# Optimization experiments

Measured on AMD Instinct MI355X. Metric: run time of the kernel, lower is better.

## Reference

```python
import jax, jax.numpy as jnp
import numpy as np

D_MODEL = 1024


def setup_inputs() -> dict:
    key = jax.random.key(0)
    kx, kq, kk, kv = jax.random.split(key, 4)
    x = jax.random.normal(kx, (4, 2048, D_MODEL), dtype=jnp.float32)
    s = 1.0 / np.sqrt(D_MODEL)
    # torch nn.Linear weight is [out, in]; y = x @ W.T
    Wq = jax.random.normal(kq, (D_MODEL, D_MODEL), dtype=jnp.float32) * s
    Wk = jax.random.normal(kk, (D_MODEL, D_MODEL), dtype=jnp.float32) * s
    Wv = jax.random.normal(kv, (D_MODEL, D_MODEL), dtype=jnp.float32) * s
    return {"x": x, "Wq": Wq, "Wk": Wk, "Wv": Wv}


def reference(x, Wq, Wk, Wv):
    # Linear projections (no bias): [b, s, d]
    Q = jnp.einsum("bsd,ed->bse", x, Wq)
    K = jnp.einsum("bsd,ed->bse", x, Wk)
    V = jnp.einsum("bsd,ed->bse", x, Wv)
    d_k = Q.shape[-1]
    scores = jnp.einsum("bqd,bkd->bqk", Q, K) / jnp.sqrt(jnp.asarray(d_k, Q.dtype))
    weights = jax.nn.softmax(scores, axis=-1)
    return jnp.einsum("bqk,bkd->bqd", weights, V)
```

## Files before the change

### kernel.cpp

```cpp
#include <hip/hip_runtime.h>
#include <hip/hip_bf16.h>

using bf16 = __hip_bfloat16;
typedef __attribute__((ext_vector_type(8))) short short8;
typedef __attribute__((ext_vector_type(16))) float f32x16;

__global__ __launch_bounds__(256) void cast_all(const float* __restrict__ x,
                                                const float* __restrict__ Wq,
                                                const float* __restrict__ Wk,
                                                const float* __restrict__ Wv,
                                                bf16* __restrict__ xb, bf16* __restrict__ Wb) {
  const int b = blockIdx.x;
  const float* src;
  bf16* dst;
  if (b < 8192) {
    src = x + (size_t)b * 1024;
    dst = xb + (size_t)b * 1024;
  } else if (b < 9216) {
    src = Wq + (size_t)(b - 8192) * 1024;
    dst = Wb + (size_t)(b - 8192) * 1024;
  } else if (b < 10240) {
    src = Wk + (size_t)(b - 9216) * 1024;
    dst = Wb + (size_t)(b - 8192) * 1024;
  } else {
    src = Wv + (size_t)(b - 10240) * 1024;
    dst = Wb + (size_t)(b - 8192) * 1024;
  }
  const int i = threadIdx.x * 4;
  const float4 f = *(const float4*)(src + i);
  bf16 h[4];
  h[0] = __float2bfloat16(f.x);
  h[1] = __float2bfloat16(f.y);
  h[2] = __float2bfloat16(f.z);
  h[3] = __float2bfloat16(f.w);
  *(uint2*)(dst + i) = *(const uint2*)h;
}

template <int BK, int SMEM_BYTES, class Epi>
__device__ __forceinline__ void gemm_nt(const bf16* __restrict__ A, const bf16* __restrict__ B,
                                        int lda, int ldb, int K, int m0, int n0, Epi epi) {
  constexpr int KS = BK / 16;
  constexpr int CPR = BK / 8;
  constexpr int SH = (BK == 32) ? 2 : 3;
  constexpr int N_INSTR = 128 * CPR / 256;
  constexpr int BUFB = 128 * BK * 2 * 2;
  static_assert(2 * BUFB <= SMEM_BYTES, "need two staging buffers");
  __shared__ char smem[SMEM_BYTES];
  const int t = threadIdx.x;
  const int lane = t & 63;
  const int wave = t >> 6;
  const int wm = (wave >> 1) * 64;
  const int wn = (wave & 1) * 64;

  f32x16 acc[2][2];
#pragma unroll
  for (int i = 0; i < 2; ++i)
#pragma unroll
    for (int j = 0; j < 2; ++j)
#pragma unroll
      for (int r = 0; r < 16; ++r) acc[i][j][r] = 0.f;

  const bf16* gA[N_INSTR];
  const bf16* gB[N_INSTR];
#pragma unroll
  for (int j = 0; j < N_INSTR; ++j) {
    const int slot = j * 256 + t;
    const int row = slot >> SH;
    const int f = (row + (row >> SH)) & (CPR - 1);
    const int c = ((slot & (CPR - 1)) ^ f) << 3;
    gA[j] = A + (size_t)(m0 + row) * lda + c;
    gB[j] = B + (size_t)(n0 + row) * ldb + c;
  }

  const int rl = lane & 31;
  const int grp = lane >> 5;

  auto stage = [&](int k0, int buf) {
    char* base = smem + buf * BUFB;
    bf16* As = (bf16*)base;
    bf16* Bs = (bf16*)(base + 128 * BK * 2);
#pragma unroll
    for (int j = 0; j < N_INSTR; ++j) {
      __builtin_amdgcn_global_load_lds(
          (const __attribute__((address_space(1))) unsigned int*)(gA[j] + k0),
          (__attribute__((address_space(3))) unsigned int*)(As + (j * 256 + wave * 64) * 8), 16, 0, 0);
      __builtin_amdgcn_global_load_lds(
          (const __attribute__((address_space(1))) unsigned int*)(gB[j] + k0),
          (__attribute__((address_space(3))) unsigned int*)(Bs + (j * 256 + wave * 64) * 8), 16, 0, 0);
    }
  };

  const int NT = K / BK;

  stage(0, 0);
  stage(BK, 1);
  asm volatile("s_waitcnt vmcnt(8)" ::: "memory");
  __builtin_amdgcn_s_barrier();
  __builtin_amdgcn_sched_barrier(0);

  for (int kt = 0; kt < NT; ++kt) {
    const char* base = smem + (kt & 1) * BUFB;
    const bf16* As = (const bf16*)base;
    const bf16* Bs = (const bf16*)(base + 128 * BK * 2);

    short8 af[KS][2], bv[KS][2];
#pragma unroll
    for (int ks = 0; ks < KS; ++ks) {
      const int kb = ks * 2 + grp;
#pragma unroll
      for (int mt = 0; mt < 2; ++mt) {
        const int rowa = wm + mt * 32 + rl;
        const int fa = (rowa + (rowa >> SH)) & (CPR - 1);
        af[ks][mt] = *(const short8*)(As + rowa * BK + ((kb ^ fa) << 3));
        const int rowb = wn + mt * 32 + rl;
        const int fb = (rowb + (rowb >> SH)) & (CPR - 1);
        bv[ks][mt] = *(const short8*)(Bs + rowb * BK + ((kb ^ fb) << 3));
      }
    }
    __builtin_amdgcn_sched_barrier(0);
    asm volatile("s_waitcnt lgkmcnt(0)" ::: "memory");
    __builtin_amdgcn_sched_barrier(0);
    __builtin_amdgcn_s_barrier();
    __builtin_amdgcn_sched_barrier(0);

    if (kt + 2 < NT) stage((kt + 2) * BK, kt & 1);

    __builtin_amdgcn_s_setprio(1);
#pragma unroll
    for (int ks = 0; ks < KS; ++ks)
#pragma unroll
      for (int mt = 0; mt < 2; ++mt)
#pragma unroll
        for (int nt = 0; nt < 2; ++nt)
          acc[mt][nt] = __builtin_amdgcn_mfma_f32_32x32x16_bf16(af[ks][mt], bv[ks][nt],
                                                                acc[mt][nt], 0, 0, 0);
    __builtin_amdgcn_s_setprio(0);
    __builtin_amdgcn_sched_barrier(0);

    if (kt + 1 < NT) {
      if (kt + 2 < NT) {
        asm volatile("s_waitcnt vmcnt(8)" ::: "memory");
      } else {
        asm volatile("s_waitcnt vmcnt(0)" ::: "memory");
      }
      __builtin_amdgcn_s_barrier();
      __builtin_amdgcn_sched_barrier(0);
    }
  }
  __syncthreads();

  epi(acc, m0, n0, wm, wn, lane, wave, smem);
}

__device__ __forceinline__ int c_row(int reg, int lane) {
  return (reg & 3) + 8 * (reg >> 2) + 4 * (lane >> 5);
}

template <class F>
__device__ __forceinline__ void for_each_c(const f32x16 (&acc)[2][2], int wm, int wn, int lane,
                                           F f) {
  const int rl = lane & 31;
#pragma unroll
  for (int mt = 0; mt < 2; ++mt)
#pragma unroll
    for (int nt = 0; nt < 2; ++nt)
#pragma unroll
      for (int reg = 0; reg < 16; ++reg)
        f(wm + mt * 32 + c_row(reg, lane), wn + nt * 32 + rl, acc[mt][nt][reg]);
}

__global__ __launch_bounds__(256) void proj_kernel(const bf16* __restrict__ xb,
                                                   const bf16* __restrict__ Wb,
                                                   bf16* __restrict__ Qb, bf16* __restrict__ Kb,
                                                   bf16* __restrict__ Vt) {
  const int id = blockIdx.y * 24 + blockIdx.x;
  const int g = id & 7, s = id >> 3;
  const int m0 = (g * 8 + (s & 7)) * 128;
  const int n0 = (s >> 3) * 128;
  gemm_nt<64, 65536>(xb, Wb, 1024, 1024, 1024, m0, n0,
             [=](const f32x16 (&acc)[2][2], int m0, int n0, int wm, int wn, int lane, int wave,
                 char* smem) {
    if (n0 < 2048) {
      bf16* dst = (n0 < 1024) ? Qb : Kb;
      const int nb = (n0 < 1024) ? n0 : (n0 - 1024);
      for_each_c(acc, wm, wn, lane, [&](int m, int n, float v) {
        dst[(size_t)(m0 + m) * 1024 + nb + n] = __float2bfloat16(v);
      });
    } else {
      bf16* T = (bf16*)(smem) + wave * 2304;
      const int rl = lane & 31;
      const int g4 = 4 * (lane >> 5);
      const int mbase = m0 + wm;
      const int bb = mbase >> 11;
      const int sbase = mbase & 2047;
      const int nvbase = n0 - 2048 + wn;
#pragma unroll
      for (int p = 0; p < 2; ++p) {
#pragma unroll
        for (int mt = 0; mt < 2; ++mt)
#pragma unroll
          for (int q = 0; q < 4; ++q) {
            bf16 h4[4];
#pragma unroll
            for (int r = 0; r < 4; ++r) h4[r] = __float2bfloat16(acc[mt][p][4 * q + r]);
            *(uint2*)(T + rl * 72 + mt * 32 + 8 * q + g4) = *(const uint2*)h4;
          }
        asm volatile("s_waitcnt lgkmcnt(0)" ::: "memory");
#pragma unroll
        for (int i = 0; i < 4; ++i) {
          const int nl = i * 8 + (lane >> 3);
          const int ml = (lane & 7) * 8;
          const short8 val = *(const short8*)(T + nl * 72 + ml);
          *(short8*)(Vt + ((size_t)bb * 1024 + nvbase + p * 32 + nl) * 2048 + sbase + ml) = val;
        }
        asm volatile("s_waitcnt lgkmcnt(0)" ::: "memory");
      }
    }
  });
}

__global__ __launch_bounds__(256) void qk_exp_kernel(const bf16* __restrict__ Qb,
                                                     const bf16* __restrict__ Kb,
                                                     bf16* __restrict__ E,
                                                     float* __restrict__ Lpart) {
  const int z = blockIdx.z;
  const int id2 = blockIdx.y * 16 + blockIdx.x;
  const int g = id2 & 7, s = id2 >> 3;
  const int m0 = ((g & 3) * 4 + (s & 3)) * 128;
  const int n0 = ((g >> 2) * 8 + (s >> 2)) * 128;
  const bf16* A = Qb + (size_t)z * 2048 * 1024;
  const bf16* B = Kb + (size_t)z * 2048 * 1024;
  bf16* Ez = E + (size_t)z * 2048 * 2048;
  float* Lz = Lpart + (size_t)z * 16 * 2048;
  gemm_nt<64, 65536>(A, B, 1024, 1024, 1024, m0, n0,
             [=](const f32x16 (&acc)[2][2], int m0, int n0, int wm, int wn, int lane, int wave,
                 char* smem) {
    float* Lp = (float*)smem;
    const int rl = lane & 31;
#pragma unroll
    for (int mt = 0; mt < 2; ++mt)
#pragma unroll
      for (int reg = 0; reg < 16; ++reg) {
        const int mr = wm + mt * 32 + c_row(reg, lane);
        float s2 = 0.f;
#pragma unroll
        for (int nt = 0; nt < 2; ++nt) {
          const float e = __expf(acc[mt][nt][reg] * 0.03125f);
          Ez[(size_t)(m0 + mr) * 2048 + n0 + wn + nt * 32 + rl] = __float2bfloat16(e);
          s2 += e;
        }
        s2 += __shfl_xor(s2, 1, 64);
        s2 += __shfl_xor(s2, 2, 64);
        s2 += __shfl_xor(s2, 4, 64);
        s2 += __shfl_xor(s2, 8, 64);
        s2 += __shfl_xor(s2, 16, 64);
        if (rl == 0) Lp[mr * 2 + (wave & 1)] = s2;
      }
    __syncthreads();
    const int t = threadIdx.x;
    if (t < 128) Lz[(n0 >> 7) * 2048 + m0 + t] = Lp[t * 2 + 0] + Lp[t * 2 + 1];
  });
}

__global__ __launch_bounds__(256) void pv_kernel(const bf16* __restrict__ E,
                                                 const bf16* __restrict__ Vt,
                                                 const float* __restrict__ Lpart,
                                                 float* __restrict__ out) {
  const int z = blockIdx.z;
  const int id2 = blockIdx.y * 8 + blockIdx.x;
  const int g = id2 & 7, s = id2 >> 3;
  const int m0 = ((g & 3) * 4 + (s & 3)) * 128;
  const int n0 = ((g >> 2) * 4 + (s >> 2)) * 128;
  const bf16* A = E + (size_t)z * 2048 * 2048;
  const bf16* B = Vt + (size_t)z * 1024 * 2048;
  const float* Lz = Lpart + (size_t)z * 16 * 2048;
  float* oz = out + (size_t)z * 2048 * 1024;
  gemm_nt<64, 65536>(A, B, 2048, 2048, 2048, m0, n0,
             [=](const f32x16 (&acc)[2][2], int m0, int n0, int wm, int wn, int lane, int wave,
                 char* smem) {
    float* Lsm = (float*)smem;
    const int t = threadIdx.x;
    if (t < 128) {
      float s2 = 0.f;
#pragma unroll
      for (int i = 0; i < 16; ++i) s2 += Lz[(size_t)i * 2048 + m0 + t];
      Lsm[t] = 1.f / s2;
    }
    __syncthreads();
    const int rl = lane & 31;
#pragma unroll
    for (int mt = 0; mt < 2; ++mt)
#pragma unroll
      for (int reg = 0; reg < 16; ++reg) {
        const int ml = wm + mt * 32 + c_row(reg, lane);
        const float il = Lsm[ml];
#pragma unroll
        for (int nt = 0; nt < 2; ++nt)
          oz[(size_t)(m0 + ml) * 1024 + n0 + wn + nt * 32 + rl] = acc[mt][nt][reg] * il;
      }
  });
}

extern "C" void kernel_launch(void* const* d_in, const int* in_sizes, int n_in,
                              void* d_out, int out_size, void* d_ws, size_t ws_size,
                              hipStream_t stream) {
  const float* x = (const float*)d_in[0];
  const float* Wq = (const float*)d_in[1];
  const float* Wk = (const float*)d_in[2];
  const float* Wv = (const float*)d_in[3];
  float* out = (float*)d_out;

  char* w = (char*)d_ws;
  bf16* xb = (bf16*)w; w += (size_t)8192 * 1024 * 2;
  bf16* Wb = (bf16*)w; w += (size_t)3072 * 1024 * 2;
  bf16* Qb = (bf16*)w; w += (size_t)8192 * 1024 * 2;
  bf16* Kb = (bf16*)w; w += (size_t)8192 * 1024 * 2;
  bf16* Vt = (bf16*)w; w += (size_t)8192 * 1024 * 2;
  bf16* E  = (bf16*)w; w += (size_t)4 * 2048 * 2048 * 2;
  float* Lpart = (float*)w; w += (size_t)4 * 16 * 2048 * 4;

  cast_all<<<11264, 256, 0, stream>>>(x, Wq, Wk, Wv, xb, Wb);

  proj_kernel<<<dim3(24, 64), 256, 0, stream>>>(xb, Wb, Qb, Kb, Vt);

  qk_exp_kernel<<<dim3(16, 16, 4), 256, 0, stream>>>(Qb, Kb, E, Lpart);

  pv_kernel<<<dim3(8, 16, 4), 256, 0, stream>>>(E, Vt, Lpart, out);
}
```

Before: 240.7 us.

## Shrink GEMM K-tile to 32 with single-barrier double buffering and occupancy 4

Hardcodes the shared GEMM core to BK=32 with two 16KB LDS slots. It also replaces the two-stage-ahead prefetch, which had split vmcnt waits and two barriers per iteration, with a one-ahead prefetch issued right after the fragment loads and followed by a full vmcnt(0) wait and a single barrier. All three GEMM kernels now request four blocks per CU via launch_bounds, which the smaller LDS footprint makes possible. The aim is to hide latency through occupancy rather than deep in-block prefetch, at the cost of shorter K steps, more barriers per unit of work, and less prefetch distance per block.

Result: slower. 248.5 us (+3.3%).

```diff
diff --git a/kernel.cpp b/kernel.cpp
--- a/kernel.cpp
+++ b/kernel.cpp
@@ -36,16 +36,15 @@
   *(uint2*)(dst + i) = *(const uint2*)h;
 }
 
-template <int BK, int SMEM_BYTES, class Epi>
+template <class Epi>
 __device__ __forceinline__ void gemm_nt(const bf16* __restrict__ A, const bf16* __restrict__ B,
                                         int lda, int ldb, int K, int m0, int n0, Epi epi) {
-  constexpr int KS = BK / 16;
-  constexpr int CPR = BK / 8;
-  constexpr int SH = (BK == 32) ? 2 : 3;
-  constexpr int N_INSTR = 128 * CPR / 256;
-  constexpr int BUFB = 128 * BK * 2 * 2;
-  static_assert(2 * BUFB <= SMEM_BYTES, "need two staging buffers");
-  __shared__ char smem[SMEM_BYTES];
+  constexpr int BK = 32;
+  constexpr int CPR = 4;
+  constexpr int SH = 2;
+  constexpr int N_INSTR = 2;
+  constexpr int SLOT = 128 * BK * 2 * 2;
+  __shared__ char smem[2 * SLOT];
   const int t = threadIdx.x;
   const int lane = t & 63;
   const int wave = t >> 6;
@@ -75,10 +74,11 @@
   const int rl = lane & 31;
   const int grp = lane >> 5;
 
-  auto stage = [&](int k0, int buf) {
-    char* base = smem + buf * BUFB;
+  auto stage = [&](int kt) {
+    char* base = smem + (kt & 1) * SLOT;
     bf16* As = (bf16*)base;
     bf16* Bs = (bf16*)(base + 128 * BK * 2);
+    const int k0 = kt * BK;
 #pragma unroll
     for (int j = 0; j < N_INSTR; ++j) {
       __builtin_amdgcn_global_load_lds(
@@ -90,22 +90,21 @@
     }
   };
 
-  const int NT = K / BK;
-
-  stage(0, 0);
-  stage(BK, 1);
-  asm volatile("s_waitcnt vmcnt(8)" ::: "memory");
+  const int NT = K >> 5;
+
+  stage(0);
+  asm volatile("s_waitcnt vmcnt(0)" ::: "memory");
   __builtin_amdgcn_s_barrier();
   __builtin_amdgcn_sched_barrier(0);
 
   for (int kt = 0; kt < NT; ++kt) {
-    const char* base = smem + (kt & 1) * BUFB;
+    const char* base = smem + (kt & 1) * SLOT;
     const bf16* As = (const bf16*)base;
     const bf16* Bs = (const bf16*)(base + 128 * BK * 2);
 
-    short8 af[KS][2], bv[KS][2];
-#pragma unroll
-    for (int ks = 0; ks < KS; ++ks) {
+    short8 af[2][2], bv[2][2];
+#pragma unroll
+    for (int ks = 0; ks < 2; ++ks) {
       const int kb = ks * 2 + grp;
 #pragma unroll
       for (int mt = 0; mt < 2; ++mt) {
@@ -117,17 +116,14 @@
         bv[ks][mt] = *(const short8*)(Bs + rowb * BK + ((kb ^ fb) << 3));
       }
     }
+    if (kt + 1 < NT) stage(kt + 1);
+
     __builtin_amdgcn_sched_barrier(0);
     asm volatile("s_waitcnt lgkmcnt(0)" ::: "memory");
     __builtin_amdgcn_sched_barrier(0);
-    __builtin_amdgcn_s_barrier();
-    __builtin_amdgcn_sched_barrier(0);
-
-    if (kt + 2 < NT) stage((kt + 2) * BK, kt & 1);
-
     __builtin_amdgcn_s_setprio(1);
 #pragma unroll
-    for (int ks = 0; ks < KS; ++ks)
+    for (int ks = 0; ks < 2; ++ks)
 #pragma unroll
       for (int mt = 0; mt < 2; ++mt)
 #pragma unroll
@@ -136,16 +132,9 @@
                                                                 acc[mt][nt], 0, 0, 0);
     __builtin_amdgcn_s_setprio(0);
     __builtin_amdgcn_sched_barrier(0);
-
-    if (kt + 1 < NT) {
-      if (kt + 2 < NT) {
-        asm volatile("s_waitcnt vmcnt(8)" ::: "memory");
-      } else {
-        asm volatile("s_waitcnt vmcnt(0)" ::: "memory");
-      }
-      __builtin_amdgcn_s_barrier();
-      __builtin_amdgcn_sched_barrier(0);
-    }
+    asm volatile("s_waitcnt vmcnt(0)" ::: "memory");
+    __builtin_amdgcn_s_barrier();
+    __builtin_amdgcn_sched_barrier(0);
   }
   __syncthreads();
 
@@ -169,17 +158,18 @@
         f(wm + mt * 32 + c_row(reg, lane), wn + nt * 32 + rl, acc[mt][nt][reg]);
 }
 
-__global__ __launch_bounds__(256) void proj_kernel(const bf16* __restrict__ xb,
-                                                   const bf16* __restrict__ Wb,
-                                                   bf16* __restrict__ Qb, bf16* __restrict__ Kb,
-                                                   bf16* __restrict__ Vt) {
+__global__ __launch_bounds__(256, 4) void proj_kernel(const bf16* __restrict__ xb,
+                                                      const bf16* __restrict__ Wb,
+                                                      bf16* __restrict__ Qb,
+                                                      bf16* __restrict__ Kb,
+                                                      bf16* __restrict__ Vt) {
   const int id = blockIdx.y * 24 + blockIdx.x;
   const int g = id & 7, s = id >> 3;
   const int m0 = (g * 8 + (s & 7)) * 128;
   const int n0 = (s >> 3) * 128;
-  gemm_nt<64, 65536>(xb, Wb, 1024, 1024, 1024, m0, n0,
-             [=](const f32x16 (&acc)[2][2], int m0, int n0, int wm, int wn, int lane, int wave,
-                 char* smem) {
+  gemm_nt(xb, Wb, 1024, 1024, 1024, m0, n0,
+          [=](const f32x16 (&acc)[2][2], int m0, int n0, int wm, int wn, int lane, int wave,
+              char* smem) {
     if (n0 < 2048) {
       bf16* dst = (n0 < 1024) ? Qb : Kb;
       const int nb = (n0 < 1024) ? n0 : (n0 - 1024);
@@ -219,10 +209,10 @@
   });
 }
 
-__global__ __launch_bounds__(256) void qk_exp_kernel(const bf16* __restrict__ Qb,
-                                                     const bf16* __restrict__ Kb,
-                                                     bf16* __restrict__ E,
-                                                     float* __restrict__ Lpart) {
+__global__ __launch_bounds__(256, 4) void qk_exp_kernel(const bf16* __restrict__ Qb,
+                                                        const bf16* __restrict__ Kb,
+                                                        bf16* __restrict__ E,
+                                                        float* __restrict__ Lpart) {
   const int z = blockIdx.z;
   const int id2 = blockIdx.y * 16 + blockIdx.x;
   const int g = id2 & 7, s = id2 >> 3;
@@ -232,9 +222,9 @@
   const bf16* B = Kb + (size_t)z * 2048 * 1024;
   bf16* Ez = E + (size_t)z * 2048 * 2048;
   float* Lz = Lpart + (size_t)z * 16 * 2048;
-  gemm_nt<64, 65536>(A, B, 1024, 1024, 1024, m0, n0,
-             [=](const f32x16 (&acc)[2][2], int m0, int n0, int wm, int wn, int lane, int wave,
-                 char* smem) {
+  gemm_nt(A, B, 1024, 1024, 1024, m0, n0,
+          [=](const f32x16 (&acc)[2][2], int m0, int n0, int wm, int wn, int lane, int wave,
+              char* smem) {
     float* Lp = (float*)smem;
     const int rl = lane & 31;
 #pragma unroll
@@ -262,10 +252,10 @@
   });
 }
 
-__global__ __launch_bounds__(256) void pv_kernel(const bf16* __restrict__ E,
-                                                 const bf16* __restrict__ Vt,
-                                                 const float* __restrict__ Lpart,
-                                                 float* __restrict__ out) {
+__global__ __launch_bounds__(256, 4) void pv_kernel(const bf16* __restrict__ E,
+                                                    const bf16* __restrict__ Vt,
+                                                    const float* __restrict__ Lpart,
+                                                    float* __restrict__ out) {
   const int z = blockIdx.z;
   const int id2 = blockIdx.y * 8 + blockIdx.x;
   const int g = id2 & 7, s = id2 >> 3;
@@ -275,9 +265,9 @@
   const bf16* B = Vt + (size_t)z * 1024 * 2048;
   const float* Lz = Lpart + (size_t)z * 16 * 2048;
   float* oz = out + (size_t)z * 2048 * 1024;
-  gemm_nt<64, 65536>(A, B, 2048, 2048, 2048, m0, n0,
-             [=](const f32x16 (&acc)[2][2], int m0, int n0, int wm, int wn, int lane, int wave,
-                 char* smem) {
+  gemm_nt(A, B, 2048, 2048, 2048, m0, n0,
+          [=](const f32x16 (&acc)[2][2], int m0, int n0, int wm, int wn, int lane, int wave,
+              char* smem) {
     float* Lsm = (float*)smem;
     const int t = threadIdx.x;
     if (t < 128) {
```
